# Kernel optimization log

Measured on AMD Instinct MI355X. Metric: run time of the kernel, lower is better.

Reference implementation:

```python
import jax, jax.numpy as jnp
import numpy as np

B, T, E = 64, 1024, 128          # batch, max_len, embedding_size
C, F = 5, 64                     # context_len, convolutional_filters
H = C // 2                       # half-window


def setup_inputs() -> dict:
    key = jax.random.key(0)
    k1, k2 = jax.random.split(key)
    x = jax.random.normal(k1, (B, T, E), dtype=jnp.float32)
    # Conv2d(1, F, (E*C, 1)) weight, flattened: W[f, k] with k = c*E + e
    # (context windows are concatenated embedding vectors, disc = -H..H)
    W = jax.random.normal(k2, (F, C * E), dtype=jnp.float32) * 0.05
    b = jnp.zeros((F,), dtype=jnp.float32)
    return {"x": x, "W": W, "b": b}


def reference(x, W, b):
    # sentence_to_Z_vector: zero-pad H positions on each side, then for each
    # position t concatenate embeddings of t-H .. t+H  -> [B, T, C*E]
    Bx, Tx, Ex = x.shape
    xp = jnp.pad(x, ((0, 0), (H, H), (0, 0)))
    # stack C shifted views (C is a small constant, loop is over kernel taps)
    Z = jnp.stack([xp[:, i:i + Tx] for i in range(C)], axis=2)  # [B, T, C, E]
    Z = Z.reshape(Bx, Tx, C * Ex)                               # [B, T, C*E]
    # degenerate full-height Conv2d == per-position matmul -> [B, F, T]
    out = jnp.einsum('btk,fk->bft', Z, W) + b[None, :, None]
    return out
```

## Files before the change

### kernel.cpp

```cpp
#include <hip/hip_runtime.h>
#include <stdint.h>

#define Bdim 64
#define Tdim 1024
#define Edim 128
#define Cdim 5
#define Fdim 64
#define Hpad 2
#define Kdim (Cdim * Edim)

#define TTILE 64
#define XROWS (TTILE + Cdim - 1)
#define LDSTR (Edim + 8)

typedef __attribute__((ext_vector_type(8))) short short8;
typedef __attribute__((ext_vector_type(4))) float float4v;
typedef __attribute__((ext_vector_type(4))) unsigned short ushort4v;

__device__ __forceinline__ unsigned short f2bf(float f) {
    union { float f; uint32_t u; } v; v.f = f;
    uint32_t u = v.u;
    u += 0x7fffu + ((u >> 16) & 1u);
    return (unsigned short)(u >> 16);
}

__global__ void convert_W(const float* __restrict__ W, unsigned short* __restrict__ Wbf) {
    int i = blockIdx.x * 256 + threadIdx.x;
    if (i >= (Fdim * Kdim) / 4) return;
    const int e0 = i * 4;
    const int f  = e0 / Kdim;
    const int k  = e0 % Kdim;
    const int c    = k / Edim;
    const int kin  = k % Edim;
    const int kk   = kin / 32;
    const int q8   = kin % 32;
    const int quad = q8 / 8;
    const int j0   = q8 % 8;
    float4v v = ((const float4v*)W)[i];
    ushort4v o = { f2bf(v.x), f2bf(v.y), f2bf(v.z), f2bf(v.w) };
    const int dst = (((c * 4 + kk) * 4 + (f >> 4)) * 4 + quad) * 128 + (f & 15) * 8 + j0;
    *(ushort4v*)&Wbf[dst] = o;
}

__global__ __launch_bounds__(256, 4)
void qa_cnn_main(const float* __restrict__ x, const unsigned short* __restrict__ Wbf,
                 const float* __restrict__ bias, float* __restrict__ out) {
    __shared__ __align__(16) unsigned short sX[XROWS * LDSTR];

    const int tid = threadIdx.x;
    const int tt  = blockIdx.x;
    const int b   = blockIdx.y;
    const int t0  = tt * TTILE;

    {
        const int nslots = XROWS * (Edim / 4);
        for (int idx = tid; idx < nslots; idx += 256) {
            const int row = idx >> 5;
            const int c4  = idx & 31;
            const int gt  = t0 - Hpad + row;
            float4v v = {0.f, 0.f, 0.f, 0.f};
            if (gt >= 0 && gt < Tdim) {
                v = *(const float4v*)(x + ((size_t)b * Tdim + gt) * Edim + c4 * 4);
            }
            ushort4v o = { f2bf(v.x), f2bf(v.y), f2bf(v.z), f2bf(v.w) };
            *(ushort4v*)&sX[row * LDSTR + c4 * 4] = o;
        }
    }

    const int wave = tid >> 6;
    const int lane = tid & 63;
    const int m16  = lane & 15;
    const int quad = lane >> 4;

    const unsigned short* wfrag = Wbf + wave * 512 + quad * 128 + m16 * 8;

    float4v acc[4];
    #pragma unroll
    for (int mt = 0; mt < 4; ++mt) acc[mt] = (float4v){0.f, 0.f, 0.f, 0.f};

    __syncthreads();

    #pragma unroll
    for (int c = 0; c < Cdim; ++c) {
        short8 bfrag[4];
        #pragma unroll
        for (int kk = 0; kk < 4; ++kk)
            bfrag[kk] = *(const short8*)(wfrag + (c * 4 + kk) * 2048);

        #pragma unroll
        for (int kk = 0; kk < 4; ++kk) {
            const int kcol = kk * 32 + quad * 8;
            #pragma unroll
            for (int mt = 0; mt < 4; ++mt) {
                const short8 a = *(const short8*)&sX[(c + mt * 16 + m16) * LDSTR + kcol];
                acc[mt] = __builtin_amdgcn_mfma_f32_16x16x32_bf16(a, bfrag[kk], acc[mt], 0, 0, 0);
            }
        }
    }

    const int f  = wave * 16 + m16;
    const float bv = bias[f];
    float* orow = out + ((size_t)b * Fdim + f) * Tdim + t0 + quad * 4;
    #pragma unroll
    for (int mt = 0; mt < 4; ++mt) {
        float4v v = acc[mt];
        v.x += bv; v.y += bv; v.z += bv; v.w += bv;
        *(float4v*)(orow + mt * 16) = v;
    }
}

extern "C" void kernel_launch(void* const* d_in, const int* in_sizes, int n_in,
                              void* d_out, int out_size, void* d_ws, size_t ws_size,
                              hipStream_t stream) {
    const float* x    = (const float*)d_in[0];
    const float* W    = (const float*)d_in[1];
    const float* bias = (const float*)d_in[2];
    float* out = (float*)d_out;
    unsigned short* Wbf = (unsigned short*)d_ws;

    convert_W<<<dim3((Fdim * Kdim / 4 + 255) / 256), dim3(256), 0, stream>>>(W, Wbf);
    qa_cnn_main<<<dim3(Tdim / TTILE, Bdim), dim3(256), 0, stream>>>(x, Wbf, bias, out);
}
```

Baseline: 88.72 us.

## Fuse weight conversion into main kernel and prefetch per-tap weights

Drops the separate convert_W launch. Each wave now reads fp32 weights straight from the original layout and converts them to bf16 in registers. The x tile loads are batched into registers before the LDS stores, and the next tap's weights are prefetched while the current tap's MFMAs run. This removes one kernel launch and its serialization, but adds redundant weight conversion in all 1024 blocks and higher register pressure.

```diff
diff --git a/kernel.cpp b/kernel.cpp
--- a/kernel.cpp
+++ b/kernel.cpp
@@ -24,26 +24,15 @@
     return (unsigned short)(u >> 16);
 }
 
-__global__ void convert_W(const float* __restrict__ W, unsigned short* __restrict__ Wbf) {
-    int i = blockIdx.x * 256 + threadIdx.x;
-    if (i >= (Fdim * Kdim) / 4) return;
-    const int e0 = i * 4;
-    const int f  = e0 / Kdim;
-    const int k  = e0 % Kdim;
-    const int c    = k / Edim;
-    const int kin  = k % Edim;
-    const int kk   = kin / 32;
-    const int q8   = kin % 32;
-    const int quad = q8 / 8;
-    const int j0   = q8 % 8;
-    float4v v = ((const float4v*)W)[i];
-    ushort4v o = { f2bf(v.x), f2bf(v.y), f2bf(v.z), f2bf(v.w) };
-    const int dst = (((c * 4 + kk) * 4 + (f >> 4)) * 4 + quad) * 128 + (f & 15) * 8 + j0;
-    *(ushort4v*)&Wbf[dst] = o;
+__device__ __forceinline__ short8 cvt8(float4v a, float4v b) {
+    union { unsigned short s[8]; short8 v; } u;
+    u.s[0] = f2bf(a.x); u.s[1] = f2bf(a.y); u.s[2] = f2bf(a.z); u.s[3] = f2bf(a.w);
+    u.s[4] = f2bf(b.x); u.s[5] = f2bf(b.y); u.s[6] = f2bf(b.z); u.s[7] = f2bf(b.w);
+    return u.v;
 }
 
 __global__ __launch_bounds__(256, 4)
-void qa_cnn_main(const float* __restrict__ x, const unsigned short* __restrict__ Wbf,
+void qa_cnn_main(const float* __restrict__ x, const float* __restrict__ W,
                  const float* __restrict__ bias, float* __restrict__ out) {
     __shared__ __align__(16) unsigned short sX[XROWS * LDSTR];
 
@@ -52,27 +41,45 @@
     const int b   = blockIdx.y;
     const int t0  = tt * TTILE;
 
-    {
-        const int nslots = XROWS * (Edim / 4);
-        for (int idx = tid; idx < nslots; idx += 256) {
-            const int row = idx >> 5;
-            const int c4  = idx & 31;
-            const int gt  = t0 - Hpad + row;
-            float4v v = {0.f, 0.f, 0.f, 0.f};
-            if (gt >= 0 && gt < Tdim) {
-                v = *(const float4v*)(x + ((size_t)b * Tdim + gt) * Edim + c4 * 4);
-            }
-            ushort4v o = { f2bf(v.x), f2bf(v.y), f2bf(v.z), f2bf(v.w) };
-            *(ushort4v*)&sX[row * LDSTR + c4 * 4] = o;
-        }
-    }
-
     const int wave = tid >> 6;
     const int lane = tid & 63;
     const int m16  = lane & 15;
     const int quad = lane >> 4;
 
-    const unsigned short* wfrag = Wbf + wave * 512 + quad * 128 + m16 * 8;
+    const float* wbase = W + (size_t)(wave * 16 + m16) * Kdim + quad * 8;
+
+    float4v xv[9];
+    #pragma unroll
+    for (int i = 0; i < 9; ++i) {
+        const int idx = tid + i * 256;
+        float4v v = {0.f, 0.f, 0.f, 0.f};
+        if (idx < XROWS * (Edim / 4)) {
+            const int row = idx >> 5;
+            const int c4  = idx & 31;
+            const int gt  = t0 - Hpad + row;
+            if (gt >= 0 && gt < Tdim)
+                v = *(const float4v*)(x + ((size_t)b * Tdim + gt) * Edim + c4 * 4);
+        }
+        xv[i] = v;
+    }
+
+    float4v w0[8];
+    #pragma unroll
+    for (int kk = 0; kk < 4; ++kk) {
+        w0[kk * 2]     = *(const float4v*)(wbase + kk * 32);
+        w0[kk * 2 + 1] = *(const float4v*)(wbase + kk * 32 + 4);
+    }
+
+    #pragma unroll
+    for (int i = 0; i < 9; ++i) {
+        const int idx = tid + i * 256;
+        if (idx < XROWS * (Edim / 4)) {
+            const int row = idx >> 5;
+            const int c4  = idx & 31;
+            ushort4v o = { f2bf(xv[i].x), f2bf(xv[i].y), f2bf(xv[i].z), f2bf(xv[i].w) };
+            *(ushort4v*)&sX[row * LDSTR + c4 * 4] = o;
+        }
+    }
 
     float4v acc[4];
     #pragma unroll
@@ -80,12 +87,20 @@
 
     __syncthreads();
 
+    short8 bfrag[4];
+    #pragma unroll
+    for (int kk = 0; kk < 4; ++kk) bfrag[kk] = cvt8(w0[kk * 2], w0[kk * 2 + 1]);
+
     #pragma unroll
     for (int c = 0; c < Cdim; ++c) {
-        short8 bfrag[4];
-        #pragma unroll
-        for (int kk = 0; kk < 4; ++kk)
-            bfrag[kk] = *(const short8*)(wfrag + (c * 4 + kk) * 2048);
+        float4v wn[8];
+        if (c + 1 < Cdim) {
+            #pragma unroll
+            for (int kk = 0; kk < 4; ++kk) {
+                wn[kk * 2]     = *(const float4v*)(wbase + (c + 1) * Edim + kk * 32);
+                wn[kk * 2 + 1] = *(const float4v*)(wbase + (c + 1) * Edim + kk * 32 + 4);
+            }
+        }
 
         #pragma unroll
         for (int kk = 0; kk < 4; ++kk) {
@@ -95,6 +110,11 @@
                 const short8 a = *(const short8*)&sX[(c + mt * 16 + m16) * LDSTR + kcol];
                 acc[mt] = __builtin_amdgcn_mfma_f32_16x16x32_bf16(a, bfrag[kk], acc[mt], 0, 0, 0);
             }
+        }
+
+        if (c + 1 < Cdim) {
+            #pragma unroll
+            for (int kk = 0; kk < 4; ++kk) bfrag[kk] = cvt8(wn[kk * 2], wn[kk * 2 + 1]);
         }
     }
 
@@ -112,12 +132,11 @@
 extern "C" void kernel_launch(void* const* d_in, const int* in_sizes, int n_in,
                               void* d_out, int out_size, void* d_ws, size_t ws_size,
                               hipStream_t stream) {
+    (void)in_sizes; (void)n_in; (void)out_size; (void)d_ws; (void)ws_size;
     const float* x    = (const float*)d_in[0];
     const float* W    = (const float*)d_in[1];
     const float* bias = (const float*)d_in[2];
     float* out = (float*)d_out;
-    unsigned short* Wbf = (unsigned short*)d_ws;
 
-    convert_W<<<dim3((Fdim * Kdim / 4 + 255) / 256), dim3(256), 0, stream>>>(W, Wbf);
-    qa_cnn_main<<<dim3(Tdim / TTILE, Bdim), dim3(256), 0, stream>>>(x, Wbf, bias, out);
+    qa_cnn_main<<<dim3(Tdim / TTILE, Bdim), dim3(256), 0, stream>>>(x, W, bias, out);
 }
```

Measured after the change: 97.52 us. 1.1x slower.

## Process two time tiles per block with double-buffered LDS and register-held weights

Applied to the files above, without the earlier changes.

Each block now handles two consecutive 64-step tiles. The second tile's global loads are issued before the first tile's MFMA compute, and the results are staged through a second LDS buffer. All 20 weight fragments are loaded into registers once per block and reused for both tiles, so weight traffic is halved. Launch bounds drop to 2 blocks per SM, trading occupancy for more register use and half as many blocks, which reduces parallelism across the GPU.

```diff
diff --git a/kernel.cpp b/kernel.cpp
--- a/kernel.cpp
+++ b/kernel.cpp
@@ -12,6 +12,7 @@
 #define TTILE 64
 #define XROWS (TTILE + Cdim - 1)
 #define LDSTR (Edim + 8)
+#define NSLOT (XROWS * (Edim / 4))
 
 typedef __attribute__((ext_vector_type(8))) short short8;
 typedef __attribute__((ext_vector_type(4))) float float4v;
@@ -42,30 +43,15 @@
     *(ushort4v*)&Wbf[dst] = o;
 }
 
-__global__ __launch_bounds__(256, 4)
+__global__ __launch_bounds__(256, 2)
 void qa_cnn_main(const float* __restrict__ x, const unsigned short* __restrict__ Wbf,
                  const float* __restrict__ bias, float* __restrict__ out) {
-    __shared__ __align__(16) unsigned short sX[XROWS * LDSTR];
+    __shared__ __align__(16) unsigned short sX[2][XROWS * LDSTR];
 
     const int tid = threadIdx.x;
-    const int tt  = blockIdx.x;
+    const int blk = blockIdx.x;
     const int b   = blockIdx.y;
-    const int t0  = tt * TTILE;
-
-    {
-        const int nslots = XROWS * (Edim / 4);
-        for (int idx = tid; idx < nslots; idx += 256) {
-            const int row = idx >> 5;
-            const int c4  = idx & 31;
-            const int gt  = t0 - Hpad + row;
-            float4v v = {0.f, 0.f, 0.f, 0.f};
-            if (gt >= 0 && gt < Tdim) {
-                v = *(const float4v*)(x + ((size_t)b * Tdim + gt) * Edim + c4 * 4);
-            }
-            ushort4v o = { f2bf(v.x), f2bf(v.y), f2bf(v.z), f2bf(v.w) };
-            *(ushort4v*)&sX[row * LDSTR + c4 * 4] = o;
-        }
-    }
+    const int t0  = blk * (2 * TTILE);
 
     const int wave = tid >> 6;
     const int lane = tid & 63;
@@ -74,44 +60,95 @@
 
     const unsigned short* wfrag = Wbf + wave * 512 + quad * 128 + m16 * 8;
 
+    auto issue_loads = [&](int t0loc, float4v xv[9]) {
+        #pragma unroll
+        for (int i = 0; i < 9; ++i) {
+            const int idx = tid + i * 256;
+            float4v v = {0.f, 0.f, 0.f, 0.f};
+            if (idx < NSLOT) {
+                const int row = idx >> 5;
+                const int c4  = idx & 31;
+                const int gt  = t0loc - Hpad + row;
+                if (gt >= 0 && gt < Tdim)
+                    v = *(const float4v*)(x + ((size_t)b * Tdim + gt) * Edim + c4 * 4);
+            }
+            xv[i] = v;
+        }
+    };
+    auto write_lds = [&](unsigned short* dst, const float4v xv[9]) {
+        #pragma unroll
+        for (int i = 0; i < 9; ++i) {
+            const int idx = tid + i * 256;
+            if (idx < NSLOT) {
+                const int row = idx >> 5;
+                const int c4  = idx & 31;
+                ushort4v o = { f2bf(xv[i].x), f2bf(xv[i].y), f2bf(xv[i].z), f2bf(xv[i].w) };
+                *(ushort4v*)&dst[row * LDSTR + c4 * 4] = o;
+            }
+        }
+    };
+
+    float4v xv[9];
+    issue_loads(t0, xv);
+
+    short8 bfr[20];
+    #pragma unroll
+    for (int ck = 0; ck < 20; ++ck)
+        bfr[ck] = *(const short8*)(wfrag + ck * 2048);
+
+    write_lds(sX[0], xv);
+
+    auto compute = [&](const unsigned short* sbuf, float4v acc[4]) {
+        #pragma unroll
+        for (int c = 0; c < Cdim; ++c) {
+            #pragma unroll
+            for (int kk = 0; kk < 4; ++kk) {
+                const int kcol = kk * 32 + quad * 8;
+                #pragma unroll
+                for (int mt = 0; mt < 4; ++mt) {
+                    const short8 a = *(const short8*)&sbuf[(c + mt * 16 + m16) * LDSTR + kcol];
+                    acc[mt] = __builtin_amdgcn_mfma_f32_16x16x32_bf16(a, bfr[c * 4 + kk], acc[mt], 0, 0, 0);
+                }
+            }
+        }
+    };
+
+    const int f  = wave * 16 + m16;
+    const float bv = bias[f];
+    auto store_out = [&](const float4v acc[4], int t0loc) {
+        float* orow = out + ((size_t)b * Fdim + f) * Tdim + t0loc + quad * 4;
+        #pragma unroll
+        for (int mt = 0; mt < 4; ++mt) {
+            float4v v = acc[mt];
+            v.x += bv; v.y += bv; v.z += bv; v.w += bv;
+            *(float4v*)(orow + mt * 16) = v;
+        }
+    };
+
+    __syncthreads();
+
+    issue_loads(t0 + TTILE, xv);
+
     float4v acc[4];
     #pragma unroll
     for (int mt = 0; mt < 4; ++mt) acc[mt] = (float4v){0.f, 0.f, 0.f, 0.f};
+    compute(sX[0], acc);
+
+    write_lds(sX[1], xv);
+    store_out(acc, t0);
 
     __syncthreads();
 
     #pragma unroll
-    for (int c = 0; c < Cdim; ++c) {
-        short8 bfrag[4];
-        #pragma unroll
-        for (int kk = 0; kk < 4; ++kk)
-            bfrag[kk] = *(const short8*)(wfrag + (c * 4 + kk) * 2048);
-
-        #pragma unroll
-        for (int kk = 0; kk < 4; ++kk) {
-            const int kcol = kk * 32 + quad * 8;
-            #pragma unroll
-            for (int mt = 0; mt < 4; ++mt) {
-                const short8 a = *(const short8*)&sX[(c + mt * 16 + m16) * LDSTR + kcol];
-                acc[mt] = __builtin_amdgcn_mfma_f32_16x16x32_bf16(a, bfrag[kk], acc[mt], 0, 0, 0);
-            }
-        }
-    }
-
-    const int f  = wave * 16 + m16;
-    const float bv = bias[f];
-    float* orow = out + ((size_t)b * Fdim + f) * Tdim + t0 + quad * 4;
-    #pragma unroll
-    for (int mt = 0; mt < 4; ++mt) {
-        float4v v = acc[mt];
-        v.x += bv; v.y += bv; v.z += bv; v.w += bv;
-        *(float4v*)(orow + mt * 16) = v;
-    }
+    for (int mt = 0; mt < 4; ++mt) acc[mt] = (float4v){0.f, 0.f, 0.f, 0.f};
+    compute(sX[1], acc);
+    store_out(acc, t0 + TTILE);
 }
 
 extern "C" void kernel_launch(void* const* d_in, const int* in_sizes, int n_in,
                               void* d_out, int out_size, void* d_ws, size_t ws_size,
                               hipStream_t stream) {
+    (void)in_sizes; (void)n_in; (void)out_size; (void)ws_size;
     const float* x    = (const float*)d_in[0];
     const float* W    = (const float*)d_in[1];
     const float* bias = (const float*)d_in[2];
@@ -119,5 +156,5 @@
     unsigned short* Wbf = (unsigned short*)d_ws;
 
     convert_W<<<dim3((Fdim * Kdim / 4 + 255) / 256), dim3(256), 0, stream>>>(W, Wbf);
-    qa_cnn_main<<<dim3(Tdim / TTILE, Bdim), dim3(256), 0, stream>>>(x, Wbf, bias, out);
+    qa_cnn_main<<<dim3(Tdim / (2 * TTILE), Bdim), dim3(256), 0, stream>>>(x, Wbf, bias, out);
 }
```

New measurement: 88.39 us. No clear change (-0.4%).
